# Kernel optimization log

Hardware: AMD Instinct MI355X
Metric: run time of the kernel (lower is better)

Reference implementation:

```python
import jax, jax.numpy as jnp
import numpy as np

N_NODES = 64000
N_GRAPHS = 128


def _sage_conv(x, edge_index, Wl, Wr, b):
    # PyG SAGEConv (mean aggregator): out = lin_l(mean_{j in N(i)} x_j) + lin_r(x_i)
    src, dst = edge_index[0], edge_index[1]
    msg = x[src]                                   # [E, d] gather
    s = jax.ops.segment_sum(msg, dst, num_segments=N_NODES)          # [N, d]
    cnt = jax.ops.segment_sum(jnp.ones(src.shape, x.dtype), dst,
                              num_segments=N_NODES)[:, None]          # [N, 1]
    aggr = jnp.where(cnt > 0, s / jnp.maximum(cnt, 1.0), jnp.zeros((), x.dtype))
    return aggr @ Wl.T + x @ Wr.T + b


def setup_inputs() -> dict:
    key = jax.random.key(0)
    ks = jax.random.split(key, 9)
    E = 1024000
    x = jax.random.normal(ks[0], (N_NODES, 64), dtype=jnp.float32)
    edge_index = jax.random.randint(ks[1], (2, E), 0, N_NODES, dtype=jnp.int64)
    batch = jnp.sort(jax.random.randint(ks[2], (N_NODES,), 0, N_GRAPHS, dtype=jnp.int64))
    sc = 1.0 / np.sqrt(64.0)
    Wl = jax.random.normal(ks[3], (3, 64, 64), dtype=jnp.float32) * sc
    Wr = jax.random.normal(ks[4], (3, 64, 64), dtype=jnp.float32) * sc
    b = jax.random.normal(ks[5], (3, 64), dtype=jnp.float32) * sc
    Wl_out = jax.random.normal(ks[6], (2, 64), dtype=jnp.float32) * sc
    Wr_out = jax.random.normal(ks[7], (2, 64), dtype=jnp.float32) * sc
    b_out = jax.random.normal(ks[8], (2,), dtype=jnp.float32) * sc
    return {"x": x, "edge_index": edge_index, "batch": batch,
            "Wl": Wl, "Wr": Wr, "b": b,
            "Wl_out": Wl_out, "Wr_out": Wr_out, "b_out": b_out}


def reference(x, edge_index, batch, Wl, Wr, b, Wl_out, Wr_out, b_out):
    h = x
    for i in range(Wl.shape[0]):  # fixed n_layers=3 hidden SAGEConv layers
        h = _sage_conv(h, edge_index, Wl[i], Wr[i], b[i])
        # dropout is identity at inference
        h = jax.nn.relu(h)
    h = _sage_conv(h, edge_index, Wl_out, Wr_out, b_out)  # [N, n_classes]
    # global mean pool over graphs in the batch
    s = jax.ops.segment_sum(h, batch, num_segments=N_GRAPHS)
    cnt = jax.ops.segment_sum(jnp.ones((N_NODES,), h.dtype), batch,
                              num_segments=N_GRAPHS)[:, None]
    return s / jnp.maximum(cnt, 1.0)
```

## Files before the change

### kernel.cpp

```cpp
#include <hip/hip_runtime.h>

#define NNODES 64000
#define NGRAPHS 128
#define D 64
#define NT 250
#define ESEG 5120
#define ZG 256

typedef _Float16 half8 __attribute__((ext_vector_type(8)));
typedef float f32x4 __attribute__((ext_vector_type(4)));

__device__ __forceinline__ int lower_bound(const int* __restrict__ a, int n, int key) {
    int lo = 0, hi = n;
    while (lo < hi) {
        int mid = (lo + hi) >> 1;
        if (a[mid] < key) lo = mid + 1; else hi = mid;
    }
    return lo;
}


__global__ void tohalf_kernel(const float4* __restrict__ x, half8* __restrict__ xh, int n8,
                              const float* __restrict__ Wl, const float* __restrict__ Wr,
                              _Float16* __restrict__ Wlh, _Float16* __restrict__ Wrh,
                              int* __restrict__ ecur) {
    int i = blockIdx.x * blockDim.x + threadIdx.x;
    int st = gridDim.x * blockDim.x;
    for (; i < n8; i += st) {
        float4 a = x[2 * i], b = x[2 * i + 1];
        half8 o;
        o[0] = (_Float16)a.x; o[1] = (_Float16)a.y; o[2] = (_Float16)a.z; o[3] = (_Float16)a.w;
        o[4] = (_Float16)b.x; o[5] = (_Float16)b.y; o[6] = (_Float16)b.z; o[7] = (_Float16)b.w;
        xh[i] = o;
    }
    int j = blockIdx.x * blockDim.x + threadIdx.x;
    if (j < 3 * D * D) {
        Wlh[j] = (_Float16)Wl[j];
        Wrh[j] = (_Float16)Wr[j];
    }
    if (blockIdx.x == 0 && threadIdx.x < 256) ecur[threadIdx.x] = 0;
}

__global__ __launch_bounds__(256) void partition_kernel(
        const int* __restrict__ src, const int* __restrict__ dst, int E,
        int* __restrict__ ecur, int2* __restrict__ elist) {
    __shared__ int bcnt[256], bbase[256];
    const int U = 8;
    int tid = threadIdx.x;
    for (int base = blockIdx.x * 256 * U; base < E; base += gridDim.x * 256 * U) {
        bcnt[tid] = 0;
        __syncthreads();
        int2 ed[U]; int team[U], slot[U];
#pragma unroll
        for (int u = 0; u < U; ++u) {
            int e = base + tid + u * 256;
            team[u] = -1;
            if (e < E) {
                int s = __builtin_nontemporal_load(src + e);
                int d = __builtin_nontemporal_load(dst + e);
                ed[u] = make_int2(s, d);
                team[u] = d >> 8;
                slot[u] = atomicAdd(&bcnt[team[u]], 1);
            }
        }
        __syncthreads();
        if (bcnt[tid] > 0) bbase[tid] = atomicAdd(&ecur[tid], bcnt[tid]);
        __syncthreads();
#pragma unroll
        for (int u = 0; u < U; ++u)
            if (team[u] >= 0)
                elist[(size_t)team[u] * ESEG + bbase[team[u]] + slot[u]] = ed[u];
        __syncthreads();
    }
}

__global__ __launch_bounds__(1024) void fill_block(
        const int2* __restrict__ elist, const int* __restrict__ ecur,
        const int* __restrict__ batch,
        int* __restrict__ offs, int2* __restrict__ info, int* __restrict__ col) {
    __shared__ int lhist[256], lofs[256];
    int team = blockIdx.x;
    int t = threadIdx.x;
    int n = ecur[team];
    const int2* el = elist + (size_t)team * ESEG;

    if (t < 256) lofs[t] = (t < NT) ? ecur[t] : 0;
    __syncthreads();
    for (int off = 1; off < 256; off <<= 1) {
        int x = 0;
        if (t < 256 && t >= off) x = lofs[t - off];
        __syncthreads();
        if (t < 256) lofs[t] += x;
        __syncthreads();
    }
    int tb = (team > 0) ? lofs[team - 1] : 0;
    if (team == NT - 1 && t == 0) offs[NNODES] = lofs[NT - 1];
    __syncthreads();

    if (t < 256) lhist[t] = 0;
    __syncthreads();
    for (int e = t; e < n; e += 1024)
        atomicAdd(&lhist[el[e].y & 255], 1);
    __syncthreads();
    if (t < 256) lofs[t] = lhist[t];
    __syncthreads();
    for (int off = 1; off < 256; off <<= 1) {
        int x = 0;
        if (t < 256 && t >= off) x = lofs[t - off];
        __syncthreads();
        if (t < 256) lofs[t] += x;
        __syncthreads();
    }
    if (t < 256) {
        int v = lhist[t];
        int ex = lofs[t] - v;
        int gi = team * 256 + t;
        offs[gi] = tb + ex;
        float inv = (v > 0) ? 1.f / (float)v : 0.f;
        info[gi] = make_int2(batch[gi], __float_as_int(inv));
        lofs[t] = ex;
    }
    __syncthreads();
    for (int e = t; e < n; e += 1024) {
        int2 ed = el[e];
        int p = tb + atomicAdd(&lofs[ed.y & 255], 1);
        col[p] = ed.x;
    }
}

template <int PRJ>
__global__ __launch_bounds__(256) void layer_fused(
        const _Float16* __restrict__ h, _Float16* __restrict__ out,
        const int* __restrict__ offs, const int* __restrict__ col,
        const _Float16* __restrict__ Wlh, const _Float16* __restrict__ Wrh,
        const float* __restrict__ b,
        const float* __restrict__ Wlo, const float* __restrict__ Wro,
        float* __restrict__ z12, float* __restrict__ z34) {
    __shared__ _Float16 tile[4][16][D];
    int lane = threadIdx.x & 63;
    int w    = threadIdx.x >> 6;
    int row0 = (blockIdx.x * 4 + w) * 16;

    int ns = lane >> 3;
    int ch = lane & 7;
#pragma unroll
    for (int pass = 0; pass < 2; ++pass) {
        int i = row0 + pass * 8 + ns;
        int beg = offs[i], end = offs[i + 1];
        half8 sa = {0, 0, 0, 0, 0, 0, 0, 0};
        int e = beg;
        for (; e + 8 <= end; e += 8) {
            int c[8];
#pragma unroll
            for (int u = 0; u < 8; ++u) c[u] = col[e + u];
            half8 v[8];
#pragma unroll
            for (int u = 0; u < 8; ++u)
                v[u] = *(const half8*)(h + (size_t)c[u] * D + ch * 8);
            half8 t0 = v[0] + v[1], t1 = v[2] + v[3];
            half8 t2 = v[4] + v[5], t3 = v[6] + v[7];
            sa += (t0 + t1) + (t2 + t3);
        }
        for (; e + 4 <= end; e += 4) {
            int c0 = col[e], c1 = col[e + 1], c2 = col[e + 2], c3 = col[e + 3];
            half8 v0 = *(const half8*)(h + (size_t)c0 * D + ch * 8);
            half8 v1 = *(const half8*)(h + (size_t)c1 * D + ch * 8);
            half8 v2 = *(const half8*)(h + (size_t)c2 * D + ch * 8);
            half8 v3 = *(const half8*)(h + (size_t)c3 * D + ch * 8);
            sa += (v0 + v1) + (v2 + v3);
        }
        for (; e < end; ++e)
            sa += *(const half8*)(h + (size_t)col[e] * D + ch * 8);
        float inv = (end > beg) ? 1.f / (float)(end - beg) : 0.f;
        half8 o;
#pragma unroll
        for (int j = 0; j < 8; ++j) o[j] = (_Float16)((float)sa[j] * inv);
        *(half8*)(&tile[w][pass * 8 + ns][ch * 8]) = o;
    }

    int r = lane & 15;
    int g = lane >> 4;

    half8 bf[4][4];
#pragma unroll
    for (int kt = 0; kt < 4; ++kt) {
        const _Float16* Wm = (kt < 2) ? Wlh : Wrh;
        int kk = (kt & 1) * 32 + g * 8;
#pragma unroll
        for (int nt = 0; nt < 4; ++nt)
            bf[kt][nt] = *(const half8*)(Wm + (size_t)(nt * 16 + r) * D + kk);
    }

    f32x4 acc[4];
#pragma unroll
    for (int nt = 0; nt < 4; ++nt) {
        float bv = b[nt * 16 + r];
        acc[nt] = (f32x4){bv, bv, bv, bv};
    }

#pragma unroll
    for (int kt = 0; kt < 4; ++kt) {
        int kk = (kt & 1) * 32 + g * 8;
        half8 af;
        if (kt < 2) af = *(const half8*)(&tile[w][r][kk]);
        else        af = *(const half8*)(h + (size_t)(row0 + r) * D + kk);
#pragma unroll
        for (int nt = 0; nt < 4; ++nt)
            acc[nt] = __builtin_amdgcn_mfma_f32_16x16x32_f16(af, bf[kt][nt], acc[nt], 0, 0, 0);
    }

    if (!PRJ) {
#pragma unroll
        for (int nt = 0; nt < 4; ++nt)
#pragma unroll
            for (int q = 0; q < 4; ++q) {
                int row = row0 + g * 4 + q;
                out[(size_t)row * D + nt * 16 + r] = (_Float16)fmaxf(acc[nt][q], 0.f);
            }
    } else {
#pragma unroll
        for (int nt = 0; nt < 4; ++nt)
#pragma unroll
            for (int q = 0; q < 4; ++q)
                tile[w][g * 4 + q][nt * 16 + r] = (_Float16)fmaxf(acc[nt][q], 0.f);

        half8 pf[2];
#pragma unroll
        for (int kt = 0; kt < 2; ++kt) {
            half8 t = {0, 0, 0, 0, 0, 0, 0, 0};
            if (r < 4) {
                const float* Pr = (r < 2) ? (Wlo + r * D) : (Wro + (r - 2) * D);
                int kk = kt * 32 + g * 8;
#pragma unroll
                for (int j = 0; j < 8; ++j) t[j] = (_Float16)Pr[kk + j];
            }
            pf[kt] = t;
        }
        f32x4 az = (f32x4){0.f, 0.f, 0.f, 0.f};
#pragma unroll
        for (int kt = 0; kt < 2; ++kt) {
            half8 af = *(const half8*)(&tile[w][r][kt * 32 + g * 8]);
            az = __builtin_amdgcn_mfma_f32_16x16x32_f16(af, pf[kt], az, 0, 0, 0);
        }
#pragma unroll
        for (int q = 0; q < 4; ++q) {
            int row = row0 + g * 4 + q;
            if (r < 2)      z12[row * 2 + r]       = az[q];
            else if (r < 4) z34[row * 2 + (r - 2)] = az[q];
        }
    }
}

__global__ __launch_bounds__(256) void zpool_edge(
        const float2* __restrict__ z12, const float2* __restrict__ z34,
        const int* __restrict__ src, const int* __restrict__ dst,
        const int2* __restrict__ info, int E, float* __restrict__ pbuf) {
    __shared__ float lp[NGRAPHS * 2];
    int t = threadIdx.x;
    lp[t] = 0.f;
    __syncthreads();
    int tid = blockIdx.x * blockDim.x + t;
    int stride = gridDim.x * blockDim.x;
    for (int e = tid; e < E; e += stride) {
        int s = __builtin_nontemporal_load(src + e);
        int d = __builtin_nontemporal_load(dst + e);
        float2 z = z12[s];
        int2 nf = info[d];
        float w = __int_as_float(nf.y);
        atomicAdd(&lp[0 * NGRAPHS + nf.x], z.x * w);
        atomicAdd(&lp[1 * NGRAPHS + nf.x], z.y * w);
    }
    for (int i = tid; i < NNODES; i += stride) {
        float2 zi = z34[i];
        int g = info[i].x;
        atomicAdd(&lp[0 * NGRAPHS + g], zi.x);
        atomicAdd(&lp[1 * NGRAPHS + g], zi.y);
    }
    __syncthreads();
    pbuf[blockIdx.x * (NGRAPHS * 2) + t] = lp[t];
}

__global__ __launch_bounds__(1024) void out_kernel(
        const float* __restrict__ pbuf, const int* __restrict__ batch,
        const float* __restrict__ bo, float* __restrict__ out) {
    __shared__ float red[4][NGRAPHS * 2];
    int tid = threadIdx.x;
    int t = tid & 255;
    int q = tid >> 8;
    float s = 0.f;
    for (int k = q * (ZG / 4); k < (q + 1) * (ZG / 4); ++k)
        s += pbuf[k * (NGRAPHS * 2) + t];
    red[q][t] = s;
    __syncthreads();
    if (q == 0) {
        float v = red[0][t] + red[1][t] + red[2][t] + red[3][t];
        int j = t >> 7, g = t & 127;
        int c = lower_bound(batch, NNODES, g + 1) - lower_bound(batch, NNODES, g);
        out[g * 2 + j] = (c > 0) ? v / (float)c + bo[j] : 0.f;
    }
}


extern "C" void kernel_launch(void* const* d_in, const int* in_sizes, int n_in,
                              void* d_out, int out_size, void* d_ws, size_t ws_size,
                              hipStream_t stream) {
    const float* x    = (const float*)d_in[0];
    const int*   eidx = (const int*)d_in[1];
    const int*   batch= (const int*)d_in[2];
    const float* Wl   = (const float*)d_in[3];
    const float* Wr   = (const float*)d_in[4];
    const float* b    = (const float*)d_in[5];
    const float* Wlo  = (const float*)d_in[6];
    const float* Wro  = (const float*)d_in[7];
    const float* bo   = (const float*)d_in[8];

    int E = in_sizes[1] / 2;
    const int* src = eidx;
    const int* dst = eidx + E;

    char* ws = (char*)d_ws;
    size_t hb = (size_t)NNODES * D * 2;
    _Float16* xh   = (_Float16*)ws;
    _Float16* bufA = (_Float16*)(ws + hb);
    char* p = ws + 2 * hb;
    _Float16* Wlh  = (_Float16*)p;  p += 3 * D * D * 2;
    _Float16* Wrh  = (_Float16*)p;  p += 3 * D * D * 2;
    int*    col  = (int*)p;     p += (size_t)E * 4;
    int*    offs = (int*)p;     p += ((size_t)(NNODES + 1) * 4 + 127) / 128 * 128;
    int2*   info = (int2*)p;    p += (size_t)NNODES * 8;
    float*  z12  = (float*)p;   p += (size_t)NNODES * 8;
    float*  z34  = (float*)p;   p += (size_t)NNODES * 8;
    int*    ecur = (int*)p;     p += 1024;
    float*  pbuf = (float*)p;   p += (size_t)ZG * NGRAPHS * 2 * 4;
    int2*   elist= (int2*)p;

    tohalf_kernel<<<2000, 256, 0, stream>>>((const float4*)x, (half8*)xh, NNODES * D / 8,
                                            Wl, Wr, Wlh, Wrh, ecur);

    partition_kernel<<<512, 256, 0, stream>>>(src, dst, E, ecur, elist);
    fill_block<<<NT, 1024, 0, stream>>>(elist, ecur, batch, offs, info, col);

    layer_fused<0><<<1000, 256, 0, stream>>>(xh,   bufA, offs, col,
                                             Wlh,             Wrh,             b,
                                             nullptr, nullptr, nullptr, nullptr);
    layer_fused<0><<<1000, 256, 0, stream>>>(bufA, xh,   offs, col,
                                             Wlh + D * D,     Wrh + D * D,     b + D,
                                             nullptr, nullptr, nullptr, nullptr);
    layer_fused<1><<<1000, 256, 0, stream>>>(xh,   bufA, offs, col,
                                             Wlh + 2 * D * D, Wrh + 2 * D * D, b + 2 * D,
                                             Wlo, Wro, z12, z34);

    zpool_edge<<<ZG, 256, 0, stream>>>((const float2*)z12, (const float2*)z34,
                                       src, dst, info, E, pbuf);
    out_kernel<<<1, 1024, 0, stream>>>(pbuf, batch, bo, (float*)d_out);
}
```

Measured before the change: 146.4 us.

## Retune partition, stage edge list in LDS, and process 16 rows per gather pass

The partition kernel drops its grid-stride loop. It now runs 250 blocks of 16 edges per thread (exactly covering E), and the z-pool grid grows from 256 to 1024 groups. fill_block copies its team's edge segment into a 40KB shared buffer on the first pass, so the scatter pass reads LDS instead of global memory again. The layer gather now handles all 16 rows in a single pass with 4 lanes per row, each loading two half8 chunks, replacing two passes of 8 rows with 8 lanes per row. Risks: less parallelism per row on long neighbour lists, extra LDS use lowering fill_block occupancy, and partition correctness now depends on the grid covering E exactly.

```diff
diff --git a/kernel.cpp b/kernel.cpp
--- a/kernel.cpp
+++ b/kernel.cpp
@@ -5,7 +5,7 @@
 #define D 64
 #define NT 250
 #define ESEG 5120
-#define ZG 256
+#define ZG 1024
 
 typedef _Float16 half8 __attribute__((ext_vector_type(8)));
 typedef float f32x4 __attribute__((ext_vector_type(4)));
@@ -45,39 +45,38 @@
         const int* __restrict__ src, const int* __restrict__ dst, int E,
         int* __restrict__ ecur, int2* __restrict__ elist) {
     __shared__ int bcnt[256], bbase[256];
-    const int U = 8;
+    const int U = 16;
     int tid = threadIdx.x;
-    for (int base = blockIdx.x * 256 * U; base < E; base += gridDim.x * 256 * U) {
-        bcnt[tid] = 0;
-        __syncthreads();
-        int2 ed[U]; int team[U], slot[U];
-#pragma unroll
-        for (int u = 0; u < U; ++u) {
-            int e = base + tid + u * 256;
-            team[u] = -1;
-            if (e < E) {
-                int s = __builtin_nontemporal_load(src + e);
-                int d = __builtin_nontemporal_load(dst + e);
-                ed[u] = make_int2(s, d);
-                team[u] = d >> 8;
-                slot[u] = atomicAdd(&bcnt[team[u]], 1);
-            }
-        }
-        __syncthreads();
-        if (bcnt[tid] > 0) bbase[tid] = atomicAdd(&ecur[tid], bcnt[tid]);
-        __syncthreads();
-#pragma unroll
-        for (int u = 0; u < U; ++u)
-            if (team[u] >= 0)
-                elist[(size_t)team[u] * ESEG + bbase[team[u]] + slot[u]] = ed[u];
-        __syncthreads();
-    }
+    int base = blockIdx.x * 256 * U;
+    bcnt[tid] = 0;
+    __syncthreads();
+    int2 ed[U]; int team[U], slot[U];
+#pragma unroll
+    for (int u = 0; u < U; ++u) {
+        int e = base + tid + u * 256;
+        team[u] = -1;
+        if (e < E) {
+            int s = __builtin_nontemporal_load(src + e);
+            int d = __builtin_nontemporal_load(dst + e);
+            ed[u] = make_int2(s, d);
+            team[u] = d >> 8;
+            slot[u] = atomicAdd(&bcnt[team[u]], 1);
+        }
+    }
+    __syncthreads();
+    if (bcnt[tid] > 0) bbase[tid] = atomicAdd(&ecur[tid], bcnt[tid]);
+    __syncthreads();
+#pragma unroll
+    for (int u = 0; u < U; ++u)
+        if (team[u] >= 0)
+            elist[(size_t)team[u] * ESEG + bbase[team[u]] + slot[u]] = ed[u];
 }
 
 __global__ __launch_bounds__(1024) void fill_block(
         const int2* __restrict__ elist, const int* __restrict__ ecur,
         const int* __restrict__ batch,
         int* __restrict__ offs, int2* __restrict__ info, int* __restrict__ col) {
+    __shared__ int2 els[ESEG];
     __shared__ int lhist[256], lofs[256];
     int team = blockIdx.x;
     int t = threadIdx.x;
@@ -99,8 +98,11 @@
 
     if (t < 256) lhist[t] = 0;
     __syncthreads();
-    for (int e = t; e < n; e += 1024)
-        atomicAdd(&lhist[el[e].y & 255], 1);
+    for (int e = t; e < n; e += 1024) {
+        int2 ed = el[e];
+        els[e] = ed;
+        atomicAdd(&lhist[ed.y & 255], 1);
+    }
     __syncthreads();
     if (t < 256) lofs[t] = lhist[t];
     __syncthreads();
@@ -122,7 +124,7 @@
     }
     __syncthreads();
     for (int e = t; e < n; e += 1024) {
-        int2 ed = el[e];
+        int2 ed = els[e];
         int p = tb + atomicAdd(&lofs[ed.y & 255], 1);
         col[p] = ed.x;
     }
@@ -141,41 +143,41 @@
     int w    = threadIdx.x >> 6;
     int row0 = (blockIdx.x * 4 + w) * 16;
 
-    int ns = lane >> 3;
-    int ch = lane & 7;
-#pragma unroll
-    for (int pass = 0; pass < 2; ++pass) {
-        int i = row0 + pass * 8 + ns;
+    {
+        int ns  = lane >> 2;
+        int ch2 = lane & 3;
+        int i = row0 + ns;
         int beg = offs[i], end = offs[i + 1];
-        half8 sa = {0, 0, 0, 0, 0, 0, 0, 0};
+        half8 s0 = {0, 0, 0, 0, 0, 0, 0, 0};
+        half8 s1 = {0, 0, 0, 0, 0, 0, 0, 0};
         int e = beg;
-        for (; e + 8 <= end; e += 8) {
-            int c[8];
-#pragma unroll
-            for (int u = 0; u < 8; ++u) c[u] = col[e + u];
-            half8 v[8];
-#pragma unroll
-            for (int u = 0; u < 8; ++u)
-                v[u] = *(const half8*)(h + (size_t)c[u] * D + ch * 8);
-            half8 t0 = v[0] + v[1], t1 = v[2] + v[3];
-            half8 t2 = v[4] + v[5], t3 = v[6] + v[7];
-            sa += (t0 + t1) + (t2 + t3);
-        }
         for (; e + 4 <= end; e += 4) {
             int c0 = col[e], c1 = col[e + 1], c2 = col[e + 2], c3 = col[e + 3];
-            half8 v0 = *(const half8*)(h + (size_t)c0 * D + ch * 8);
-            half8 v1 = *(const half8*)(h + (size_t)c1 * D + ch * 8);
-            half8 v2 = *(const half8*)(h + (size_t)c2 * D + ch * 8);
-            half8 v3 = *(const half8*)(h + (size_t)c3 * D + ch * 8);
-            sa += (v0 + v1) + (v2 + v3);
-        }
-        for (; e < end; ++e)
-            sa += *(const half8*)(h + (size_t)col[e] * D + ch * 8);
+            const _Float16* r0 = h + (size_t)c0 * D + ch2 * 16;
+            const _Float16* r1 = h + (size_t)c1 * D + ch2 * 16;
+            const _Float16* r2 = h + (size_t)c2 * D + ch2 * 16;
+            const _Float16* r3 = h + (size_t)c3 * D + ch2 * 16;
+            half8 a0 = *(const half8*)r0,       a1 = *(const half8*)r1;
+            half8 a2 = *(const half8*)r2,       a3 = *(const half8*)r3;
+            half8 b0 = *(const half8*)(r0 + 8), b1 = *(const half8*)(r1 + 8);
+            half8 b2 = *(const half8*)(r2 + 8), b3 = *(const half8*)(r3 + 8);
+            s0 += (a0 + a1) + (a2 + a3);
+            s1 += (b0 + b1) + (b2 + b3);
+        }
+        for (; e < end; ++e) {
+            const _Float16* rp = h + (size_t)col[e] * D + ch2 * 16;
+            s0 += *(const half8*)rp;
+            s1 += *(const half8*)(rp + 8);
+        }
         float inv = (end > beg) ? 1.f / (float)(end - beg) : 0.f;
-        half8 o;
-#pragma unroll
-        for (int j = 0; j < 8; ++j) o[j] = (_Float16)((float)sa[j] * inv);
-        *(half8*)(&tile[w][pass * 8 + ns][ch * 8]) = o;
+        half8 o0, o1;
+#pragma unroll
+        for (int j = 0; j < 8; ++j) {
+            o0[j] = (_Float16)((float)s0[j] * inv);
+            o1[j] = (_Float16)((float)s1[j] * inv);
+        }
+        *(half8*)(&tile[w][ns][ch2 * 16])     = o0;
+        *(half8*)(&tile[w][ns][ch2 * 16 + 8]) = o1;
     }
 
     int r = lane & 15;
@@ -337,7 +339,7 @@
     tohalf_kernel<<<2000, 256, 0, stream>>>((const float4*)x, (half8*)xh, NNODES * D / 8,
                                             Wl, Wr, Wlh, Wrh, ecur);
 
-    partition_kernel<<<512, 256, 0, stream>>>(src, dst, E, ecur, elist);
+    partition_kernel<<<NT, 256, 0, stream>>>(src, dst, E, ecur, elist);
     fill_block<<<NT, 1024, 0, stream>>>(elist, ecur, batch, offs, info, col);
 
     layer_fused<0><<<1000, 256, 0, stream>>>(xh,   bufA, offs, col,
```

Measured after the change: 210.2 us. 1.44x slower.
